# Kernel tuning notes

Hardware: AMD Instinct MI355X
Metric: run time of the kernel (lower is better)

Reference implementation:

```python
import jax, jax.numpy as jnp
import numpy as np

TAU = 1.0  # FLAGS.tau


def setup_inputs() -> dict:
    key = jax.random.key(0)
    k1, k2, k3, k4 = jax.random.split(key, 4)
    B, N, E, D_in, D_out = 64, 512, 8, 64, 64
    edge_features = jax.random.normal(k1, (B, N, N, E), dtype=jnp.float32)
    x = jax.random.normal(k2, (B * N, D_in), dtype=jnp.float32)
    # glorot init for weights, normal for coef (as in source)
    lim = np.sqrt(6.0 / (D_in + D_out))
    W = jax.random.uniform(k3, (D_in, D_out), dtype=jnp.float32, minval=-lim, maxval=lim)
    coef = jax.random.normal(k4, (E, 1), dtype=jnp.float32)
    return {"edge_features": edge_features, "x": x, "W": W, "coef": coef}


def reference(edge_features, x, W, coef):
    B, N, _, E = edge_features.shape
    D_out = W.shape[1]
    # node transform: [B*N, D_in] @ [D_in, D_out]
    pre_sup = (x @ W).reshape(B, N, D_out)
    # per-edge attention score: [B,N,N,E] @ [E,1] -> [B,N,N]
    scores = jnp.einsum('bije,e->bij', edge_features, coef[:, 0])
    adj = jax.nn.softmax(scores / TAU, axis=-1)
    # preprocess_adj: add self-loops, symmetric D^-1/2 (A+I) D^-1/2.
    # Block-diagonal structure means normalization is per-graph, so we stay batched
    # instead of materializing the [B*N, B*N] block-diagonal matrix.
    adj_hat = adj + jnp.eye(N, dtype=adj.dtype)
    d_inv_sqrt = jax.lax.rsqrt(adj_hat.sum(axis=-1))  # [B,N]
    adj_norm = adj_hat * d_inv_sqrt[:, :, None] * d_inv_sqrt[:, None, :]
    # adjacency-weighted aggregation (block-diagonal matmul == batched matmul)
    out = jnp.einsum('bij,bjd->bid', adj_norm, pre_sup).reshape(B * N, D_out)
    return jax.nn.relu(out)
```

## Files before the change

### kernel.cpp

```cpp
#include <hip/hip_runtime.h>
#include <math.h>

#define B_  64
#define N_  512
#define E_  8
#define D_  64
#define RG  8
#define WV  4

typedef float f32x4 __attribute__((ext_vector_type(4)));

__global__ __launch_bounds__(256) void presup_kernel(
    const float* __restrict__ x, const float* __restrict__ W, float* __restrict__ ps)
{
    __shared__ float Wl[64 * 64];
    const int t = threadIdx.x;
#pragma unroll
    for (int i = 0; i < 4; ++i)
        ((f32x4*)Wl)[t + i * 256] = ((const f32x4*)W)[t + i * 256];
    __syncthreads();

    const int d4  = (t & 15) * 4;
    const int r   = t >> 4;
    const int row = blockIdx.x * 16 + r;
    const float* xr = x + (size_t)row * 64;

    f32x4 acc = 0.f;
#pragma unroll
    for (int k = 0; k < 64; k += 4) {
        f32x4 xv = *(const f32x4*)&xr[k];
        f32x4 w0 = *(const f32x4*)&Wl[(k + 0) * 64 + d4];
        f32x4 w1 = *(const f32x4*)&Wl[(k + 1) * 64 + d4];
        f32x4 w2 = *(const f32x4*)&Wl[(k + 2) * 64 + d4];
        f32x4 w3 = *(const f32x4*)&Wl[(k + 3) * 64 + d4];
        acc += xv.x * w0;
        acc += xv.y * w1;
        acc += xv.z * w2;
        acc += xv.w * w3;
    }
    *(f32x4*)&ps[(size_t)row * 64 + d4] = acc;
}

__global__ __launch_bounds__(256, 4) void fused_kernel(
    const float* __restrict__ edge, const float* __restrict__ coef,
    const float* __restrict__ ps, float* __restrict__ out)
{
    __shared__ alignas(16) float pl[WV][64][RG];

    const int t = threadIdx.x, w = t >> 6, l = t & 63;
    const int blk  = blockIdx.x;
    const int b    = blk >> 4;
    const int row0 = (blk & 15) * (WV * RG) + w * RG;

    const float c0 = coef[0], c1 = coef[1], c2 = coef[2], c3 = coef[3];
    const float c4 = coef[4], c5 = coef[5], c6 = coef[6], c7 = coef[7];

    const float* eb  = edge + (((size_t)b * N_ + row0) * N_ + l) * E_;
    const float* psb = ps + (size_t)b * (N_ * D_);

    float acc[RG], lsum[RG];
#pragma unroll
    for (int r = 0; r < RG; ++r) { acc[r] = 0.f; lsum[r] = 0.f; }

    for (int c = 0; c < N_ / 64; ++c) {
        const int j0 = c * 64;

        f32x4 pv0, pv1;
#pragma unroll
        for (int r = 0; r < RG; ++r) {
            const f32x4* ep = (const f32x4*)(eb + ((size_t)r * N_ + j0) * E_);
            f32x4 e0 = __builtin_nontemporal_load(ep);
            f32x4 e1 = __builtin_nontemporal_load(ep + 1);
            float s = e0.x * c0 + e0.y * c1 + e0.z * c2 + e0.w * c3
                    + e1.x * c4 + e1.y * c5 + e1.z * c6 + e1.w * c7;
            float p = __expf(s);
            lsum[r] += p;
            if (r < 4) pv0[r] = p; else pv1[r - 4] = p;
        }
        *(f32x4*)&pl[w][l][0] = pv0;
        *(f32x4*)&pl[w][l][4] = pv1;

#pragma unroll 8
        for (int j = 0; j < 64; ++j) {
            f32x4 pa = *(const f32x4*)&pl[w][j][0];
            f32x4 pb = *(const f32x4*)&pl[w][j][4];
            float v  = psb[(size_t)(j0 + j) * D_ + l];
            acc[0] += pa.x * v;  acc[1] += pa.y * v;
            acc[2] += pa.z * v;  acc[3] += pa.w * v;
            acc[4] += pb.x * v;  acc[5] += pb.y * v;
            acc[6] += pb.z * v;  acc[7] += pb.w * v;
        }
    }

#pragma unroll
    for (int r = 0; r < RG; ++r) {
        float s = lsum[r];
#pragma unroll
        for (int off = 32; off; off >>= 1) s += __shfl_xor(s, off, 64);
        const int row = row0 + r;
        const float self = psb[(size_t)row * D_ + l];
        const float val  = 0.5f * (acc[r] / s + self);
        __builtin_nontemporal_store(fmaxf(val, 0.f),
                                    &out[((size_t)b * N_ + row) * D_ + l]);
    }
}

extern "C" void kernel_launch(void* const* d_in, const int* in_sizes, int n_in,
                              void* d_out, int out_size, void* d_ws, size_t ws_size,
                              hipStream_t stream) {
    const float* edge = (const float*)d_in[0];
    const float* x    = (const float*)d_in[1];
    const float* W    = (const float*)d_in[2];
    const float* coef = (const float*)d_in[3];
    float* out = (float*)d_out;
    float* ps  = (float*)d_ws;

    presup_kernel<<<(B_ * N_) / 16, 256, 0, stream>>>(x, W, ps);
    fused_kernel<<<B_ * N_ / (WV * RG), 256, 0, stream>>>(edge, coef, ps, out);
}
```

Baseline: 150.9 us.

## Split fused kernel into bf16 score pass and MFMA aggregation pass

Replaces the single fused softmax-plus-aggregation kernel with three stages. The presup kernel also writes a transposed, permuted bf16 copy of pre_sup, and a score kernel writes the row-normalized softmax probabilities as bf16 to workspace. An aggregation kernel then does the batched adjacency matmul with bf16 MFMA 16x16x32 instructions instead of scalar FP32 FMAs out of LDS. This removes the FP32 inner-product bottleneck but adds a 32 MB bf16 intermediate round trip through memory, an extra launch, and bf16 rounding error in the attention weights and features.

```diff
diff --git a/kernel.cpp b/kernel.cpp
--- a/kernel.cpp
+++ b/kernel.cpp
@@ -1,17 +1,20 @@
 #include <hip/hip_runtime.h>
+#include <hip/hip_bf16.h>
 #include <math.h>
 
 #define B_  64
 #define N_  512
 #define E_  8
 #define D_  64
-#define RG  8
-#define WV  4
 
 typedef float f32x4 __attribute__((ext_vector_type(4)));
+typedef short s16x8 __attribute__((ext_vector_type(8)));
+typedef unsigned short u16;
+
 
 __global__ __launch_bounds__(256) void presup_kernel(
-    const float* __restrict__ x, const float* __restrict__ W, float* __restrict__ ps)
+    const float* __restrict__ x, const float* __restrict__ W,
+    float* __restrict__ ps, u16* __restrict__ psT)
 {
     __shared__ float Wl[64 * 64];
     const int t = threadIdx.x;
@@ -39,70 +42,90 @@
         acc += xv.w * w3;
     }
     *(f32x4*)&ps[(size_t)row * 64 + d4] = acc;
+
+    const int b  = row >> 9, rb = row & 511;
+    const int q  = ((rb & 63) << 3) | (rb >> 6);
+#pragma unroll
+    for (int i = 0; i < 4; ++i) {
+        union { __hip_bfloat16 h; u16 u; } cv;
+        cv.h = __float2bfloat16(acc[i]);
+        psT[((size_t)b * 64 + d4 + i) * 512 + q] = cv.u;
+    }
 }
 
-__global__ __launch_bounds__(256, 4) void fused_kernel(
+__global__ __launch_bounds__(256) void score_kernel(
     const float* __restrict__ edge, const float* __restrict__ coef,
-    const float* __restrict__ ps, float* __restrict__ out)
+    u16* __restrict__ Pn)
 {
-    __shared__ alignas(16) float pl[WV][64][RG];
-
     const int t = threadIdx.x, w = t >> 6, l = t & 63;
-    const int blk  = blockIdx.x;
-    const int b    = blk >> 4;
-    const int row0 = (blk & 15) * (WV * RG) + w * RG;
+    const size_t row = (size_t)blockIdx.x * 4 + w;
+    const float* eb = edge + row * (size_t)(N_ * E_) + (size_t)l * 8;
 
     const float c0 = coef[0], c1 = coef[1], c2 = coef[2], c3 = coef[3];
     const float c4 = coef[4], c5 = coef[5], c6 = coef[6], c7 = coef[7];
 
-    const float* eb  = edge + (((size_t)b * N_ + row0) * N_ + l) * E_;
-    const float* psb = ps + (size_t)b * (N_ * D_);
-
-    float acc[RG], lsum[RG];
+    f32x4 e0[8], e1[8];
 #pragma unroll
-    for (int r = 0; r < RG; ++r) { acc[r] = 0.f; lsum[r] = 0.f; }
-
-    for (int c = 0; c < N_ / 64; ++c) {
-        const int j0 = c * 64;
-
-        f32x4 pv0, pv1;
-#pragma unroll
-        for (int r = 0; r < RG; ++r) {
-            const f32x4* ep = (const f32x4*)(eb + ((size_t)r * N_ + j0) * E_);
-            f32x4 e0 = __builtin_nontemporal_load(ep);
-            f32x4 e1 = __builtin_nontemporal_load(ep + 1);
-            float s = e0.x * c0 + e0.y * c1 + e0.z * c2 + e0.w * c3
-                    + e1.x * c4 + e1.y * c5 + e1.z * c6 + e1.w * c7;
-            float p = __expf(s);
-            lsum[r] += p;
-            if (r < 4) pv0[r] = p; else pv1[r - 4] = p;
-        }
-        *(f32x4*)&pl[w][l][0] = pv0;
-        *(f32x4*)&pl[w][l][4] = pv1;
-
-#pragma unroll 8
-        for (int j = 0; j < 64; ++j) {
-            f32x4 pa = *(const f32x4*)&pl[w][j][0];
-            f32x4 pb = *(const f32x4*)&pl[w][j][4];
-            float v  = psb[(size_t)(j0 + j) * D_ + l];
-            acc[0] += pa.x * v;  acc[1] += pa.y * v;
-            acc[2] += pa.z * v;  acc[3] += pa.w * v;
-            acc[4] += pb.x * v;  acc[5] += pb.y * v;
-            acc[6] += pb.z * v;  acc[7] += pb.w * v;
-        }
+    for (int k = 0; k < 8; ++k) {
+        const f32x4* p = (const f32x4*)(eb + (size_t)k * 512);
+        e0[k] = __builtin_nontemporal_load(p);
+        e1[k] = __builtin_nontemporal_load(p + 1);
     }
 
+    float pv[8];
+    float sum = 0.f;
 #pragma unroll
-    for (int r = 0; r < RG; ++r) {
-        float s = lsum[r];
+    for (int k = 0; k < 8; ++k) {
+        float s = e0[k].x * c0 + e0[k].y * c1 + e0[k].z * c2 + e0[k].w * c3
+                + e1[k].x * c4 + e1[k].y * c5 + e1[k].z * c6 + e1[k].w * c7;
+        pv[k] = __expf(s);
+        sum += pv[k];
+    }
 #pragma unroll
-        for (int off = 32; off; off >>= 1) s += __shfl_xor(s, off, 64);
-        const int row = row0 + r;
-        const float self = psb[(size_t)row * D_ + l];
-        const float val  = 0.5f * (acc[r] / s + self);
-        __builtin_nontemporal_store(fmaxf(val, 0.f),
-                                    &out[((size_t)b * N_ + row) * D_ + l]);
+    for (int off = 32; off; off >>= 1) sum += __shfl_xor(sum, off, 64);
+    const float rs = 1.f / sum;
+
+    union { u16 us[8]; f32x4 v; } pk;
+#pragma unroll
+    for (int k = 0; k < 8; ++k) {
+        union { __hip_bfloat16 h; u16 u; } cv;
+        cv.h = __float2bfloat16(pv[k] * rs);
+        pk.us[k] = cv.u;
     }
+    __builtin_nontemporal_store(pk.v, (f32x4*)(Pn + row * N_ + (size_t)l * 8));
+}
+
+__global__ __launch_bounds__(256) void agg_kernel(
+    const u16* __restrict__ Pn, const u16* __restrict__ psT,
+    const float* __restrict__ ps, float* __restrict__ out)
+{
+    const int t = threadIdx.x, w = t >> 6, l = t & 63;
+    const int blk = blockIdx.x;
+    const int b   = blk >> 5;
+    const int qq  = blk & 31;
+    const int m0  = (qq >> 3) * 16;
+    const int n0  = ((qq & 7) * 4 + w) * 16;
+
+    const u16* Ab = psT + ((size_t)b * 64 + m0 + (l & 15)) * 512 + (l >> 4) * 8;
+    const u16* Bb = Pn  + ((size_t)b * N_ + n0 + (l & 15)) * 512 + (l >> 4) * 8;
+
+    f32x4 acc = {0.f, 0.f, 0.f, 0.f};
+#pragma unroll
+    for (int k0 = 0; k0 < 512; k0 += 32) {
+        s16x8 a  = *(const s16x8*)(Ab + k0);
+        s16x8 bb = *(const s16x8*)(Bb + k0);
+        acc = __builtin_amdgcn_mfma_f32_16x16x32_bf16(a, bb, acc, 0, 0, 0);
+    }
+
+    const int i  = n0 + (l & 15);
+    const int d0 = m0 + (l >> 4) * 4;
+    const size_t rowoff = ((size_t)b * N_ + i) * 64 + d0;
+    f32x4 self = *(const f32x4*)&ps[rowoff];
+    f32x4 r;
+#pragma unroll
+    for (int c = 0; c < 4; ++c)
+        r[c] = fmaxf(0.5f * (acc[c] + self[c]), 0.f);
+    __builtin_nontemporal_store(r, (f32x4*)&out[rowoff]);
 }
 
 extern "C" void kernel_launch(void* const* d_in, const int* in_sizes, int n_in,
@@ -113,8 +136,13 @@
     const float* W    = (const float*)d_in[2];
     const float* coef = (const float*)d_in[3];
     float* out = (float*)d_out;
-    float* ps  = (float*)d_ws;
 
-    presup_kernel<<<(B_ * N_) / 16, 256, 0, stream>>>(x, W, ps);
-    fused_kernel<<<B_ * N_ / (WV * RG), 256, 0, stream>>>(edge, coef, ps, out);
+    char* ws = (char*)d_ws;
+    float* ps  = (float*)ws;
+    u16*   psT = (u16*)(ws + (8u << 20));
+    u16*   Pn  = (u16*)(ws + (12u << 20));
+
+    presup_kernel<<<(B_ * N_) / 16, 256, 0, stream>>>(x, W, ps, psT);
+    score_kernel<<<(B_ * N_) / 4, 256, 0, stream>>>(edge, coef, Pn);
+    agg_kernel<<<B_ * 32, 256, 0, stream>>>(Pn, psT, ps, out);
 }
```

Measured after the change: 183.6 us. +21.6%, slower.

## Coalesce edge loads with lane shuffles and pack softmax weights as bf16 in LDS

Applied to the files above, without the earlier changes.

Each lane now reads contiguous 16-byte chunks, so a wave's edge loads for one row are fully coalesced across 64 edges. Each half-dot over 4 features is combined with a neighbour lane by xor-shuffle and then redistributed so every lane gets its own edge score. The unnormalized exp weights are rounded to bf16 and packed into LDS, halving LDS traffic in the aggregation loop. This costs extra shuffles and unpack ALU, drops the nontemporal hint, and adds bf16 rounding error to the attention weights.

```diff
diff --git a/kernel.cpp b/kernel.cpp
--- a/kernel.cpp
+++ b/kernel.cpp
@@ -9,6 +9,17 @@
 #define WV  4
 
 typedef float f32x4 __attribute__((ext_vector_type(4)));
+typedef unsigned int u32;
+typedef u32 u32x4 __attribute__((ext_vector_type(4)));
+
+__device__ __forceinline__ u32 pack_bf16x2(float a, float b) {
+    u32 ua = __float_as_uint(a), ub = __float_as_uint(b);
+    ua = (ua + 0x7fffu + ((ua >> 16) & 1u)) >> 16;
+    ub = (ub + 0x7fffu + ((ub >> 16) & 1u)) >> 16;
+    return ua | (ub << 16);
+}
+__device__ __forceinline__ float bf16lo(u32 w) { return __uint_as_float(w << 16); }
+__device__ __forceinline__ float bf16hi(u32 w) { return __uint_as_float(w & 0xffff0000u); }
 
 __global__ __launch_bounds__(256) void presup_kernel(
     const float* __restrict__ x, const float* __restrict__ W, float* __restrict__ ps)
@@ -45,17 +56,20 @@
     const float* __restrict__ edge, const float* __restrict__ coef,
     const float* __restrict__ ps, float* __restrict__ out)
 {
-    __shared__ alignas(16) float pl[WV][64][RG];
+    __shared__ alignas(16) u32 plb[WV][64][4];
 
     const int t = threadIdx.x, w = t >> 6, l = t & 63;
     const int blk  = blockIdx.x;
     const int b    = blk >> 4;
     const int row0 = (blk & 15) * (WV * RG) + w * RG;
 
-    const float c0 = coef[0], c1 = coef[1], c2 = coef[2], c3 = coef[3];
-    const float c4 = coef[4], c5 = coef[5], c6 = coef[6], c7 = coef[7];
+    f32x4 cA, cB;
+    cA.x = coef[0]; cA.y = coef[1]; cA.z = coef[2]; cA.w = coef[3];
+    cB.x = coef[4]; cB.y = coef[5]; cB.z = coef[6]; cB.w = coef[7];
+    const f32x4 ch = (l & 1) ? cB : cA;
+    const int src = (2 * l) & 63;
 
-    const float* eb  = edge + (((size_t)b * N_ + row0) * N_ + l) * E_;
+    const float* ebl = edge + ((size_t)b * N_ + row0) * (size_t)(N_ * E_) + 4 * l;
     const float* psb = ps + (size_t)b * (N_ * D_);
 
     float acc[RG], lsum[RG];
@@ -63,32 +77,38 @@
     for (int r = 0; r < RG; ++r) { acc[r] = 0.f; lsum[r] = 0.f; }
 
     for (int c = 0; c < N_ / 64; ++c) {
-        const int j0 = c * 64;
-
-        f32x4 pv0, pv1;
+        float prow[RG];
 #pragma unroll
         for (int r = 0; r < RG; ++r) {
-            const f32x4* ep = (const f32x4*)(eb + ((size_t)r * N_ + j0) * E_);
-            f32x4 e0 = __builtin_nontemporal_load(ep);
-            f32x4 e1 = __builtin_nontemporal_load(ep + 1);
-            float s = e0.x * c0 + e0.y * c1 + e0.z * c2 + e0.w * c3
-                    + e1.x * c4 + e1.y * c5 + e1.z * c6 + e1.w * c7;
-            float p = __expf(s);
+            const float* rp = ebl + (size_t)r * (N_ * E_) + c * 512;
+            f32x4 eA = *(const f32x4*)rp;
+            f32x4 eB = *(const f32x4*)(rp + 256);
+            float dA = eA.x * ch.x + eA.y * ch.y + eA.z * ch.z + eA.w * ch.w;
+            float dB = eB.x * ch.x + eB.y * ch.y + eB.z * ch.z + eB.w * ch.w;
+            dA += __shfl_xor(dA, 1, 64);
+            dB += __shfl_xor(dB, 1, 64);
+            float sA = __shfl(dA, src, 64);
+            float sB = __shfl(dB, src, 64);
+            float p  = __expf((l < 32) ? sA : sB);
+            prow[r] = p;
             lsum[r] += p;
-            if (r < 4) pv0[r] = p; else pv1[r - 4] = p;
         }
-        *(f32x4*)&pl[w][l][0] = pv0;
-        *(f32x4*)&pl[w][l][4] = pv1;
+        u32x4 pk;
+        pk.x = pack_bf16x2(prow[0], prow[1]);
+        pk.y = pack_bf16x2(prow[2], prow[3]);
+        pk.z = pack_bf16x2(prow[4], prow[5]);
+        pk.w = pack_bf16x2(prow[6], prow[7]);
+        *(u32x4*)&plb[w][l][0] = pk;
 
+        const int j0 = c * 64;
 #pragma unroll 8
         for (int j = 0; j < 64; ++j) {
-            f32x4 pa = *(const f32x4*)&pl[w][j][0];
-            f32x4 pb = *(const f32x4*)&pl[w][j][4];
+            u32x4 pw = *(const u32x4*)&plb[w][j][0];
             float v  = psb[(size_t)(j0 + j) * D_ + l];
-            acc[0] += pa.x * v;  acc[1] += pa.y * v;
-            acc[2] += pa.z * v;  acc[3] += pa.w * v;
-            acc[4] += pb.x * v;  acc[5] += pb.y * v;
-            acc[6] += pb.z * v;  acc[7] += pb.w * v;
+            acc[0] += bf16lo(pw.x) * v;  acc[1] += bf16hi(pw.x) * v;
+            acc[2] += bf16lo(pw.y) * v;  acc[3] += bf16hi(pw.y) * v;
+            acc[4] += bf16lo(pw.z) * v;  acc[5] += bf16hi(pw.z) * v;
+            acc[6] += bf16lo(pw.w) * v;  acc[7] += bf16hi(pw.w) * v;
         }
     }
 
```

Measured after the change: 146.1 us. -3.2%, faster.
